# Kernel optimization log

Hardware: AMD Instinct MI355X
Metric: run time of the kernel (lower is better)

The kernel has to match this reference:

```python
import jax, jax.numpy as jnp
import numpy as np

B, S, D = 4, 4096, 768

def setup_inputs() -> dict:
    key = jax.random.key(0)
    kx, kq, kk, kv = jax.random.split(key, 4)
    x = jax.random.normal(kx, (B, S, D), dtype=jnp.float32)
    Wq = jax.random.normal(kq, (D, D), dtype=jnp.float32) * (D ** -0.5)
    Wk = jax.random.normal(kk, (D, D), dtype=jnp.float32) * (D ** -0.5)
    Wv = jax.random.normal(kv, (D, D), dtype=jnp.float32) * (D ** -0.5)
    return {"x": x, "Wq": Wq, "Wk": Wk, "Wv": Wv}

def reference(x, Wq, Wk, Wv):
    # q,k,v: [B,S,D]  (Linear with no bias)
    q = x @ Wq
    k = x @ Wk
    v = x @ Wv
    # full N x N causal score matrix, as in the original module
    scores = jnp.einsum('bqd,bkd->bqk', q, k)  # [B,S,S]
    seq = scores.shape[1]
    causal_mask = jnp.triu(jnp.ones((seq, seq), dtype=bool), k=1)  # True above diagonal
    scores = jnp.where(causal_mask[None, :, :], -jnp.inf, scores)
    scale = jnp.asarray(k.shape[-1], scores.dtype) ** 0.5
    weights = jax.nn.softmax(scores / scale, axis=-1)  # [B,S,S]
    # dropout p=0.0 -> identity (deterministic reference)
    context = jnp.einsum('bqk,bkd->bqd', weights, v)  # [B,S,D]
    return context
```

## Files before the change

### kernel.cpp

```cpp
#include <hip/hip_runtime.h>
#include <hip/hip_bf16.h>

typedef __attribute__((ext_vector_type(8))) _Float16 half8_t;
typedef __attribute__((ext_vector_type(4))) _Float16 half4_t;
typedef __attribute__((ext_vector_type(4))) float float4_t;

#define D_DIM 768
#define S_DIM 4096
#define B_DIM 4
#define M_DIM (B_DIM * S_DIM)
#define SD ((size_t)S_DIM * D_DIM)

#define GLOAD_LDS16(g, s)                                      \
  __builtin_amdgcn_global_load_lds(                            \
      (const __attribute__((address_space(1))) void*)(g),      \
      (__attribute__((address_space(3))) void*)(s), 16, 0, 0)

__device__ __forceinline__ float4_t mfma16(half8_t a, half8_t b, float4_t c) {
  return __builtin_amdgcn_mfma_f32_16x16x32_f16(a, b, c, 0, 0, 0);
}

__global__ __launch_bounds__(256) void cvt_x_kernel(const float* __restrict__ in,
                                                    _Float16* __restrict__ out, int n) {
  int i = (blockIdx.x * 256 + threadIdx.x) * 4;
  if (i < n) {
    float4 v = *(const float4*)(in + i);
    half4_t o;
    o.x = (_Float16)v.x; o.y = (_Float16)v.y; o.z = (_Float16)v.z; o.w = (_Float16)v.w;
    *(half4_t*)(out + i) = o;
  }
}

__global__ __launch_bounds__(256) void transpose_w_kernel(const float* __restrict__ W0,
                                                          const float* __restrict__ W1,
                                                          const float* __restrict__ W2,
                                                          _Float16* __restrict__ WT) {
  const float* W = (blockIdx.z == 0) ? W0 : (blockIdx.z == 1) ? W1 : W2;
  _Float16* o = WT + (size_t)blockIdx.z * D_DIM * D_DIM;
  __shared__ _Float16 tile[64][68];
  int k0 = blockIdx.x * 64, n0 = blockIdx.y * 64;
#pragma unroll
  for (int i = 0; i < 16; ++i) {
    int idx = threadIdx.x + i * 256;
    int r = idx >> 6, c = idx & 63;
    tile[r][c] = (_Float16)W[(size_t)(k0 + r) * D_DIM + n0 + c];
  }
  __syncthreads();
#pragma unroll
  for (int i = 0; i < 16; ++i) {
    int idx = threadIdx.x + i * 256;
    int r = idx >> 6, c = idx & 63;
    o[(size_t)(n0 + r) * D_DIM + k0 + c] = tile[c][r];
  }
}

template <bool SWAP>
__device__ __forceinline__ void core128(const _Float16* __restrict__ Ag,
                                        const _Float16* __restrict__ Bg,
                                        int lda, int ldb, int nt,
                                        char* lds, float4_t (&acc)[4][4]) {
  const int tid = threadIdx.x;
  const int w = tid >> 6, l = tid & 63;
  const int wr = w >> 1, wc = w & 1;
  const int l15 = l & 15, l4 = l >> 4;

  int sA[4], sB[4], sDst[4];
#pragma unroll
  for (int i = 0; i < 4; ++i) {
    int L = i * 256 + tid;
    int row = L >> 3, u = L & 7;
    int usw = u ^ (row & 7);
    sA[i] = row * lda + usw * 8;
    sB[i] = row * ldb + usw * 8;
    sDst[i] = (i * 256 + (tid & ~63)) * 16;
  }

  int aOff[2][4], bOff[2][4];
#pragma unroll
  for (int ks = 0; ks < 2; ++ks) {
#pragma unroll
    for (int i = 0; i < 4; ++i) {
      int ar = wr * 64 + i * 16 + l15;
      aOff[ks][i] = ar * 128 + (((ks * 4 + l4) ^ (ar & 7)) * 16);
      int br = wc * 64 + i * 16 + l15;
      bOff[ks][i] = 16384 + br * 128 + (((ks * 4 + l4) ^ (br & 7)) * 16);
    }
  }

#pragma unroll 1
  for (int kt = 0; kt < nt; ++kt) {
#pragma unroll
    for (int i = 0; i < 4; ++i)
      GLOAD_LDS16(Ag + (size_t)kt * 64 + sA[i], lds + sDst[i]);
#pragma unroll
    for (int i = 0; i < 4; ++i)
      GLOAD_LDS16(Bg + (size_t)kt * 64 + sB[i], lds + 16384 + sDst[i]);
    __syncthreads();
#pragma unroll
    for (int ks = 0; ks < 2; ++ks) {
      half8_t af[4], bf[4];
#pragma unroll
      for (int ni = 0; ni < 4; ++ni) bf[ni] = *(const half8_t*)(lds + bOff[ks][ni]);
#pragma unroll
      for (int mi = 0; mi < 4; ++mi) af[mi] = *(const half8_t*)(lds + aOff[ks][mi]);
      __builtin_amdgcn_s_setprio(1);
#pragma unroll
      for (int mi = 0; mi < 4; ++mi)
#pragma unroll
        for (int ni = 0; ni < 4; ++ni) {
          if (SWAP)
            acc[mi][ni] = mfma16(bf[ni], af[mi], acc[mi][ni]);
          else
            acc[mi][ni] = mfma16(af[mi], bf[ni], acc[mi][ni]);
        }
      __builtin_amdgcn_s_setprio(0);
    }
    __syncthreads();
  }
}

__global__ __launch_bounds__(256) void proj8_kernel(const _Float16* __restrict__ xh,
                                                    const _Float16* __restrict__ WT,
                                                    _Float16* __restrict__ qkv,
                                                    _Float16* __restrict__ vt) {
  __shared__ __align__(16) char lds[32768];
  const int bid = blockIdx.x;
  const int wid = (bid & 7) * 288 + (bid >> 3);
  const int rbg = wid / 18;
  const int rem = wid % 18;
  const int z = rem / 6;
  const int cb = rem % 6;

  const _Float16* Ag = xh + (size_t)rbg * 128 * D_DIM;
  const _Float16* Bg = WT + (size_t)z * D_DIM * D_DIM + (size_t)cb * 128 * D_DIM;
  float4_t acc[4][4];
#pragma unroll
  for (int a = 0; a < 4; ++a)
#pragma unroll
    for (int b = 0; b < 4; ++b) acc[a][b] = (float4_t){0.f, 0.f, 0.f, 0.f};

  const int tid = threadIdx.x;
  const int w = tid >> 6, l = tid & 63;
  const int wr = w >> 1, wc = w & 1;
  const int l15 = l & 15, l4 = l >> 4;

  if (z < 2) {
    core128<false>(Ag, Bg, D_DIM, D_DIM, 12, lds, acc);
    _Float16* C = qkv + (size_t)z * M_DIM * D_DIM;
#pragma unroll
    for (int mi = 0; mi < 4; ++mi)
#pragma unroll
      for (int ni = 0; ni < 4; ++ni) {
        int col = cb * 128 + wc * 64 + ni * 16 + l15;
#pragma unroll
        for (int j = 0; j < 4; ++j) {
          int row = rbg * 128 + wr * 64 + mi * 16 + l4 * 4 + j;
          C[(size_t)row * D_DIM + col] = (_Float16)acc[mi][ni][j];
        }
      }
  } else {
    core128<true>(Ag, Bg, D_DIM, D_DIM, 12, lds, acc);
#pragma unroll
    for (int mi = 0; mi < 4; ++mi) {
      int scol = rbg * 128 + wr * 64 + mi * 16 + l15;
      int bb = scol >> 12;
      int sl = scol & 4095;
      _Float16* vtb = vt + (size_t)bb * SD;
#pragma unroll
      for (int ni = 0; ni < 4; ++ni) {
#pragma unroll
        for (int j = 0; j < 4; ++j) {
          int drow = cb * 128 + wc * 64 + ni * 16 + l4 * 4 + j;
          vtb[(size_t)drow * S_DIM + sl] = (_Float16)acc[mi][ni][j];
        }
      }
    }
  }
}

__global__ __launch_bounds__(256) void gemm1_8_kernel(const _Float16* __restrict__ Q,
                                                      const _Float16* __restrict__ K,
                                                      _Float16* __restrict__ P,
                                                      float* __restrict__ rp) {
  __shared__ __align__(16) char lds[32768];
  const float SCALE = 0.036084391824351615f;
  const int bid = blockIdx.x;
  const int wid = (bid & 7) * 264 + (bid >> 3);
  const int z = wid / 528;
  const int t = wid % 528;
  int g = 0;
  while (g < 7 && (8 * (g + 1) * g + 10 * (g + 1)) <= t) ++g;
  int r = t - (8 * g * (g - 1) + 10 * g);
  int rbg, cb;
  if (r < 16 * g) {
    int cbg = r >> 4, wi = r & 15;
    rbg = 4 * g + (wi >> 2);
    cb = 4 * cbg + (wi & 3);
  } else {
    int r2 = r - 16 * g;
    const int ri[10] = {0, 1, 1, 2, 2, 2, 3, 3, 3, 3};
    const int rj[10] = {0, 0, 1, 0, 1, 2, 0, 1, 2, 3};
    rbg = 4 * g + ri[r2];
    cb = 4 * g + rj[r2];
  }

  const _Float16* Ag = Q + (size_t)z * SD + (size_t)rbg * 128 * D_DIM;
  const _Float16* Bg = K + (size_t)z * SD + (size_t)cb * 128 * D_DIM;
  float4_t acc[4][4];
#pragma unroll
  for (int a = 0; a < 4; ++a)
#pragma unroll
    for (int b = 0; b < 4; ++b) acc[a][b] = (float4_t){0.f, 0.f, 0.f, 0.f};
  core128<false>(Ag, Bg, D_DIM, D_DIM, 12, lds, acc);

  const int tid = threadIdx.x;
  const int w = tid >> 6, l = tid & 63;
  const int wr = w >> 1, wc = w & 1;
  const int l15 = l & 15, l4 = l >> 4;
  _Float16* Pz = P + (size_t)z * S_DIM * S_DIM;
  float* rpz = rp + (size_t)z * S_DIM * 64;
#pragma unroll
  for (int mi = 0; mi < 4; ++mi) {
#pragma unroll
    for (int j = 0; j < 4; ++j) {
      int row = rbg * 128 + wr * 64 + mi * 16 + l4 * 4 + j;
      float rs = 0.f;
#pragma unroll
      for (int ni = 0; ni < 4; ++ni) {
        int col = cb * 128 + wc * 64 + ni * 16 + l15;
        float v = (col <= row) ? __expf(acc[mi][ni][j] * SCALE - 4.0f) : 0.f;
        _Float16 ph = (_Float16)v;
        Pz[(size_t)row * S_DIM + col] = ph;
        rs += (float)ph;
      }
#pragma unroll
      for (int d = 1; d < 16; d <<= 1) rs += __shfl_xor(rs, d);
      if (l15 == 0) rpz[(size_t)row * 64 + cb * 2 + wc] = rs;
    }
  }
}

__global__ __launch_bounds__(256) void rsum_combine_kernel(const float* __restrict__ rp,
                                                           float* __restrict__ rsum) {
  int idx = blockIdx.x * 256 + threadIdx.x;
  int row = idx & 4095;
  int np = ((row >> 7) + 1) * 2;
  const float* p = rp + (size_t)idx * 64;
  float s = 0.f;
  for (int i = 0; i < np; ++i) s += p[i];
  rsum[idx] = s;
}

__global__ __launch_bounds__(256) void gemm2_8_kernel(const _Float16* __restrict__ P,
                                                      const _Float16* __restrict__ VT,
                                                      float* __restrict__ outp,
                                                      const float* __restrict__ rsum) {
  __shared__ __align__(16) char lds[32768];
  const int bid = blockIdx.x;
  const int g = bid / 24;
  const int q = bid % 24;
  const int rbg = 31 - g;
  const int xcd = q & 7;
  const int slot = q >> 3;
  const int z = xcd >> 1;
  const int by = (xcd & 1) * 3 + slot;
  const int nt = 2 * (rbg + 1);

  const _Float16* Ag = P + (size_t)z * S_DIM * S_DIM + (size_t)rbg * 128 * S_DIM;
  const _Float16* Bg = VT + (size_t)z * SD + (size_t)by * 128 * S_DIM;
  float4_t acc[4][4];
#pragma unroll
  for (int a = 0; a < 4; ++a)
#pragma unroll
    for (int b = 0; b < 4; ++b) acc[a][b] = (float4_t){0.f, 0.f, 0.f, 0.f};
  core128<false>(Ag, Bg, S_DIM, S_DIM, nt, lds, acc);

  const int tid = threadIdx.x;
  const int w = tid >> 6, l = tid & 63;
  const int wr = w >> 1, wc = w & 1;
  const int l15 = l & 15, l4 = l >> 4;
#pragma unroll
  for (int mi = 0; mi < 4; ++mi) {
#pragma unroll
    for (int j = 0; j < 4; ++j) {
      int row = rbg * 128 + wr * 64 + mi * 16 + l4 * 4 + j;
      float rinv = 1.0f / rsum[(size_t)z * S_DIM + row];
#pragma unroll
      for (int ni = 0; ni < 4; ++ni) {
        int col = by * 128 + wc * 64 + ni * 16 + l15;
        outp[(size_t)z * SD + (size_t)row * D_DIM + col] = acc[mi][ni][j] * rinv;
      }
    }
  }
}

extern "C" void kernel_launch(void* const* d_in, const int* in_sizes, int n_in,
                              void* d_out, int out_size, void* d_ws, size_t ws_size,
                              hipStream_t stream) {
  const float* x = (const float*)d_in[0];
  const float* Wq = (const float*)d_in[1];
  const float* Wk = (const float*)d_in[2];
  const float* Wv = (const float*)d_in[3];
  float* out = (float*)d_out;
  char* ws = (char*)d_ws;

  const size_t XH_B = (size_t)M_DIM * D_DIM * 2;
  const size_t QKV_B = 3 * XH_B;
  const size_t VT_B = XH_B;
  const size_t WT_B = (size_t)3 * D_DIM * D_DIM * 2;
  const size_t BASE_END = XH_B + QKV_B + VT_B + WT_B;

  _Float16* xh = (_Float16*)ws;
  _Float16* qkv = (_Float16*)(ws + XH_B);
  _Float16* Q = qkv;
  _Float16* K = qkv + (size_t)M_DIM * D_DIM;
  _Float16* vt = (_Float16*)(ws + XH_B + QKV_B);
  _Float16* wt = (_Float16*)(ws + XH_B + QKV_B + VT_B);

  float* rp = (float*)(ws + BASE_END);
  float* rsum = (float*)(ws + BASE_END + (size_t)4194304);
  _Float16* P = (_Float16*)(ws + BASE_END + (size_t)4259840);

  cvt_x_kernel<<<dim3(12288), dim3(256), 0, stream>>>(x, xh, M_DIM * D_DIM);
  transpose_w_kernel<<<dim3(12, 12, 3), dim3(256), 0, stream>>>(Wq, Wk, Wv, wt);
  proj8_kernel<<<dim3(2304), dim3(256), 0, stream>>>(xh, wt, qkv, vt);
  gemm1_8_kernel<<<dim3(2112), dim3(256), 0, stream>>>(Q, K, P, rp);
  rsum_combine_kernel<<<dim3(64), dim3(256), 0, stream>>>(rp, rsum);
  gemm2_8_kernel<<<dim3(768), dim3(256), 0, stream>>>(P, vt, out, rsum);
}
```

Measured before the change: 266.9 us.

## Use 256x256 tiles with 8-wave double-buffered core for projection and QK GEMMs

Adds a new GEMM core that computes 256x256 output tiles with 512 threads, staging 64-wide K slices into a 128 KB double-buffered LDS via direct global-to-LDS loads so the next slice's fetch overlaps the current slice's MFMAs. The projection and score GEMMs switch to this core, with remapped block indices, a new causal tile enumeration and an adjusted row-partial-sum layout and combine count. Larger tiles raise arithmetic intensity and cut global traffic per FLOP. In exchange, occupancy drops to one block per CU because of the LDS size, fewer blocks are launched, and causal diagonal tiles now waste more work on masked entries.

```diff
diff --git a/kernel.cpp b/kernel.cpp
--- a/kernel.cpp
+++ b/kernel.cpp
@@ -52,6 +52,103 @@
     int r = idx >> 6, c = idx & 63;
     o[(size_t)(n0 + r) * D_DIM + k0 + c] = tile[c][r];
   }
+}
+
+template <bool SWAP>
+__device__ __forceinline__ void core256p(const _Float16* __restrict__ Ag,
+                                         const _Float16* __restrict__ Bg,
+                                         int lda, int ldb, int nt,
+                                         char* lds, float4_t (&acc)[8][4]) {
+  const int tid = threadIdx.x;
+  const int w = tid >> 6, l = tid & 63;
+  const int wm = w >> 2, wn = w & 3;
+  const int l15 = l & 15, l4 = l >> 4;
+
+  int sRow[2], sU[2], sDst[2];
+#pragma unroll
+  for (int i = 0; i < 2; ++i) {
+    int L = i * 512 + tid;
+    int row = L >> 3, u = L & 7;
+    sRow[i] = row;
+    sU[i] = (u ^ (row & 7)) * 8;
+    sDst[i] = (i * 512 + (tid & ~63)) * 16;
+  }
+
+  const int a7 = l15 & 7;
+  const int kt0 = ((0 * 4 + l4) ^ a7) * 16;
+  const int kt1 = ((1 * 4 + l4) ^ a7) * 16;
+  const int aBase = (wm * 128 + l15) * 128;
+  const int bBase = 32768 + (wn * 64 + l15) * 128;
+
+#define STGP(t)                                                                 \
+  do {                                                                          \
+    char* base = lds + ((t) & 1) * 65536;                                       \
+    const _Float16* As = Ag + (size_t)(t) * 64;                                 \
+    const _Float16* Bs = Bg + (size_t)(t) * 64;                                 \
+    _Pragma("unroll") for (int i = 0; i < 2; ++i)                               \
+        GLOAD_LDS16(As + (size_t)sRow[i] * lda + sU[i], base + sDst[i]);        \
+    _Pragma("unroll") for (int i = 0; i < 2; ++i)                               \
+        GLOAD_LDS16(As + (size_t)(sRow[i] + 128) * lda + sU[i],                 \
+                    base + 16384 + sDst[i]);                                    \
+    _Pragma("unroll") for (int i = 0; i < 2; ++i)                               \
+        GLOAD_LDS16(Bs + (size_t)sRow[i] * ldb + sU[i], base + 32768 + sDst[i]);\
+    _Pragma("unroll") for (int i = 0; i < 2; ++i)                               \
+        GLOAD_LDS16(Bs + (size_t)(sRow[i] + 128) * ldb + sU[i],                 \
+                    base + 49152 + sDst[i]);                                    \
+  } while (0)
+
+  STGP(0);
+
+#pragma unroll 1
+  for (int t = 0; t < nt; ++t) {
+    asm volatile("s_waitcnt vmcnt(0)" ::: "memory");
+    __builtin_amdgcn_s_barrier();
+    __builtin_amdgcn_sched_barrier(0);
+    if (t + 1 < nt) STGP(t + 1);
+    __builtin_amdgcn_sched_barrier(0);
+
+    const char* Lb = lds + (t & 1) * 65536;
+    const char* pA0 = Lb + aBase + kt0;
+    const char* pA1 = Lb + aBase + kt1;
+    const char* pB0 = Lb + bBase + kt0;
+    const char* pB1 = Lb + bBase + kt1;
+
+    half8_t bf[4][2];
+#pragma unroll
+    for (int ni = 0; ni < 4; ++ni) {
+      bf[ni][0] = *(const half8_t*)(pB0 + ni * 2048);
+      bf[ni][1] = *(const half8_t*)(pB1 + ni * 2048);
+    }
+
+#pragma unroll
+    for (int q = 0; q < 4; ++q) {
+      if (q) {
+        __builtin_amdgcn_s_barrier();
+        __builtin_amdgcn_sched_barrier(0);
+      }
+      half8_t af[2][2];
+#pragma unroll
+      for (int di = 0; di < 2; ++di) {
+        af[di][0] = *(const half8_t*)(pA0 + (q * 2 + di) * 2048);
+        af[di][1] = *(const half8_t*)(pA1 + (q * 2 + di) * 2048);
+      }
+      __builtin_amdgcn_s_setprio(1);
+#pragma unroll
+      for (int di = 0; di < 2; ++di)
+#pragma unroll
+        for (int ni = 0; ni < 4; ++ni)
+#pragma unroll
+          for (int ks = 0; ks < 2; ++ks) {
+            if (SWAP)
+              acc[q * 2 + di][ni] = mfma16(bf[ni][ks], af[di][ks], acc[q * 2 + di][ni]);
+            else
+              acc[q * 2 + di][ni] = mfma16(af[di][ks], bf[ni][ks], acc[q * 2 + di][ni]);
+          }
+      __builtin_amdgcn_s_setprio(0);
+    }
+    __builtin_amdgcn_s_barrier();
+  }
+#undef STGP
 }
 
 template <bool SWAP>
@@ -119,50 +216,51 @@
   }
 }
 
-__global__ __launch_bounds__(256) void proj8_kernel(const _Float16* __restrict__ xh,
+__global__ __launch_bounds__(512) void proj8_kernel(const _Float16* __restrict__ xh,
                                                     const _Float16* __restrict__ WT,
                                                     _Float16* __restrict__ qkv,
                                                     _Float16* __restrict__ vt) {
-  __shared__ __align__(16) char lds[32768];
+  __shared__ __align__(16) char lds[131072];
   const int bid = blockIdx.x;
-  const int wid = (bid & 7) * 288 + (bid >> 3);
-  const int rbg = wid / 18;
+  const int wid = (bid & 7) * 72 + (bid >> 3);
+  const int rg2 = wid / 18;
   const int rem = wid % 18;
   const int z = rem / 6;
-  const int cb = rem % 6;
-
-  const _Float16* Ag = xh + (size_t)rbg * 128 * D_DIM;
-  const _Float16* Bg = WT + (size_t)z * D_DIM * D_DIM + (size_t)cb * 128 * D_DIM;
-  float4_t acc[4][4];
-#pragma unroll
-  for (int a = 0; a < 4; ++a)
+  const int cb = (rem % 6) >> 1;
+  const int rbg = rg2 * 2 + (rem & 1);
+
+  const _Float16* Ag = xh + (size_t)rbg * 256 * D_DIM;
+  const _Float16* Bg = WT + (size_t)z * D_DIM * D_DIM + (size_t)cb * 256 * D_DIM;
+  float4_t acc[8][4];
+#pragma unroll
+  for (int a = 0; a < 8; ++a)
 #pragma unroll
     for (int b = 0; b < 4; ++b) acc[a][b] = (float4_t){0.f, 0.f, 0.f, 0.f};
 
   const int tid = threadIdx.x;
   const int w = tid >> 6, l = tid & 63;
-  const int wr = w >> 1, wc = w & 1;
+  const int wr = w >> 2, wc = w & 3;
   const int l15 = l & 15, l4 = l >> 4;
 
   if (z < 2) {
-    core128<false>(Ag, Bg, D_DIM, D_DIM, 12, lds, acc);
+    core256p<false>(Ag, Bg, D_DIM, D_DIM, 12, lds, acc);
     _Float16* C = qkv + (size_t)z * M_DIM * D_DIM;
 #pragma unroll
-    for (int mi = 0; mi < 4; ++mi)
+    for (int mi = 0; mi < 8; ++mi)
 #pragma unroll
       for (int ni = 0; ni < 4; ++ni) {
-        int col = cb * 128 + wc * 64 + ni * 16 + l15;
+        int col = cb * 256 + wc * 64 + ni * 16 + l15;
 #pragma unroll
         for (int j = 0; j < 4; ++j) {
-          int row = rbg * 128 + wr * 64 + mi * 16 + l4 * 4 + j;
+          int row = rbg * 256 + wr * 128 + mi * 16 + l4 * 4 + j;
           C[(size_t)row * D_DIM + col] = (_Float16)acc[mi][ni][j];
         }
       }
   } else {
-    core128<true>(Ag, Bg, D_DIM, D_DIM, 12, lds, acc);
-#pragma unroll
-    for (int mi = 0; mi < 4; ++mi) {
-      int scol = rbg * 128 + wr * 64 + mi * 16 + l15;
+    core256p<true>(Ag, Bg, D_DIM, D_DIM, 12, lds, acc);
+#pragma unroll
+    for (int mi = 0; mi < 8; ++mi) {
+      int scol = rbg * 256 + wr * 128 + mi * 16 + l15;
       int bb = scol >> 12;
       int sl = scol & 4095;
       _Float16* vtb = vt + (size_t)bb * SD;
@@ -170,7 +268,7 @@
       for (int ni = 0; ni < 4; ++ni) {
 #pragma unroll
         for (int j = 0; j < 4; ++j) {
-          int drow = cb * 128 + wc * 64 + ni * 16 + l4 * 4 + j;
+          int drow = cb * 256 + wc * 64 + ni * 16 + l4 * 4 + j;
           vtb[(size_t)drow * S_DIM + sl] = (_Float16)acc[mi][ni][j];
         }
       }
@@ -178,19 +276,22 @@
   }
 }
 
-__global__ __launch_bounds__(256) void gemm1_8_kernel(const _Float16* __restrict__ Q,
+__global__ __launch_bounds__(512) void gemm1_8_kernel(const _Float16* __restrict__ Q,
                                                       const _Float16* __restrict__ K,
                                                       _Float16* __restrict__ P,
                                                       float* __restrict__ rp) {
-  __shared__ __align__(16) char lds[32768];
+  __shared__ __align__(16) char lds[131072];
   const float SCALE = 0.036084391824351615f;
   const int bid = blockIdx.x;
-  const int wid = (bid & 7) * 264 + (bid >> 3);
-  const int z = wid / 528;
-  const int t = wid % 528;
-  int g = 0;
-  while (g < 7 && (8 * (g + 1) * g + 10 * (g + 1)) <= t) ++g;
-  int r = t - (8 * g * (g - 1) + 10 * g);
+  const int wid = (bid & 7) * 68 + (bid >> 3);
+  const int z = wid / 136;
+  const int t = wid % 136;
+  int g, base;
+  if (t < 10) { g = 0; base = 0; }
+  else if (t < 36) { g = 1; base = 10; }
+  else if (t < 78) { g = 2; base = 36; }
+  else { g = 3; base = 78; }
+  int r = t - base;
   int rbg, cb;
   if (r < 16 * g) {
     int cbg = r >> 4, wi = r & 15;
@@ -204,30 +305,30 @@
     cb = 4 * g + rj[r2];
   }
 
-  const _Float16* Ag = Q + (size_t)z * SD + (size_t)rbg * 128 * D_DIM;
-  const _Float16* Bg = K + (size_t)z * SD + (size_t)cb * 128 * D_DIM;
-  float4_t acc[4][4];
-#pragma unroll
-  for (int a = 0; a < 4; ++a)
+  const _Float16* Ag = Q + (size_t)z * SD + (size_t)rbg * 256 * D_DIM;
+  const _Float16* Bg = K + (size_t)z * SD + (size_t)cb * 256 * D_DIM;
+  float4_t acc[8][4];
+#pragma unroll
+  for (int a = 0; a < 8; ++a)
 #pragma unroll
     for (int b = 0; b < 4; ++b) acc[a][b] = (float4_t){0.f, 0.f, 0.f, 0.f};
-  core128<false>(Ag, Bg, D_DIM, D_DIM, 12, lds, acc);
+  core256p<false>(Ag, Bg, D_DIM, D_DIM, 12, lds, acc);
 
   const int tid = threadIdx.x;
   const int w = tid >> 6, l = tid & 63;
-  const int wr = w >> 1, wc = w & 1;
+  const int wr = w >> 2, wc = w & 3;
   const int l15 = l & 15, l4 = l >> 4;
   _Float16* Pz = P + (size_t)z * S_DIM * S_DIM;
   float* rpz = rp + (size_t)z * S_DIM * 64;
 #pragma unroll
-  for (int mi = 0; mi < 4; ++mi) {
+  for (int mi = 0; mi < 8; ++mi) {
 #pragma unroll
     for (int j = 0; j < 4; ++j) {
-      int row = rbg * 128 + wr * 64 + mi * 16 + l4 * 4 + j;
+      int row = rbg * 256 + wr * 128 + mi * 16 + l4 * 4 + j;
       float rs = 0.f;
 #pragma unroll
       for (int ni = 0; ni < 4; ++ni) {
-        int col = cb * 128 + wc * 64 + ni * 16 + l15;
+        int col = cb * 256 + wc * 64 + ni * 16 + l15;
         float v = (col <= row) ? __expf(acc[mi][ni][j] * SCALE - 4.0f) : 0.f;
         _Float16 ph = (_Float16)v;
         Pz[(size_t)row * S_DIM + col] = ph;
@@ -235,7 +336,7 @@
       }
 #pragma unroll
       for (int d = 1; d < 16; d <<= 1) rs += __shfl_xor(rs, d);
-      if (l15 == 0) rpz[(size_t)row * 64 + cb * 2 + wc] = rs;
+      if (l15 == 0) rpz[(size_t)row * 64 + cb * 4 + wc] = rs;
     }
   }
 }
@@ -244,7 +345,7 @@
                                                            float* __restrict__ rsum) {
   int idx = blockIdx.x * 256 + threadIdx.x;
   int row = idx & 4095;
-  int np = ((row >> 7) + 1) * 2;
+  int np = ((row >> 8) + 1) * 4;
   const float* p = rp + (size_t)idx * 64;
   float s = 0.f;
   for (int i = 0; i < np; ++i) s += p[i];
@@ -323,8 +424,8 @@
 
   cvt_x_kernel<<<dim3(12288), dim3(256), 0, stream>>>(x, xh, M_DIM * D_DIM);
   transpose_w_kernel<<<dim3(12, 12, 3), dim3(256), 0, stream>>>(Wq, Wk, Wv, wt);
-  proj8_kernel<<<dim3(2304), dim3(256), 0, stream>>>(xh, wt, qkv, vt);
-  gemm1_8_kernel<<<dim3(2112), dim3(256), 0, stream>>>(Q, K, P, rp);
+  proj8_kernel<<<dim3(576), dim3(512), 0, stream>>>(xh, wt, qkv, vt);
+  gemm1_8_kernel<<<dim3(544), dim3(512), 0, stream>>>(Q, K, P, rp);
   rsum_combine_kernel<<<dim3(64), dim3(256), 0, stream>>>(rp, rsum);
   gemm2_8_kernel<<<dim3(768), dim3(256), 0, stream>>>(P, vt, out, rsum);
 }
```

After: 275.9 us. +3.3%, slower.
